# Kernel optimization log

Hardware: AMD Instinct MI355X
Metric: run time of the kernel (lower is better)

The kernel has to match this reference:

```python
import jax, jax.numpy as jnp
import numpy as np

N_NODES = 10000
N_EDGES = 640000
D = 128
N_LAYERS = 4


def setup_inputs() -> dict:
    key = jax.random.key(0)
    k1, k2, k3, k4, k5 = jax.random.split(key, 5)
    node_feats = jax.random.normal(k1, (N_NODES, D), dtype=jnp.float32)
    src = jax.random.randint(k2, (N_EDGES,), 0, N_NODES, dtype=jnp.int32)
    dst = jax.random.randint(k3, (N_EDGES,), 0, N_NODES, dtype=jnp.int32)
    # stacked per-layer Linear params (all layers are 128 -> 128)
    Ws = jax.random.normal(k4, (N_LAYERS, D, D), dtype=jnp.float32) / np.sqrt(D).astype(np.float32)
    bs = jax.random.normal(k5, (N_LAYERS, D), dtype=jnp.float32) * 0.01
    return {"node_feats": node_feats, "src": src, "dst": dst, "Ws": Ws, "bs": bs}


def reference(node_feats, src, dst, Ws, bs):
    # Each GCN_layer: h = Linear(x); h = sum_{u in N(v)} h_u  (copy_u/sum)
    # dgl.add_self_loop => aggregate includes the node's own h, i.e. + h.
    # activation = relu; dropout is identity in eval; no batchnorm / residual.
    def step(h, params):
        W, b = params
        hl = h @ W + b                                   # [N, D] dense GEMM
        msgs = hl[src]                                   # [E, D] gather
        agg = jax.ops.segment_sum(msgs, dst, num_segments=N_NODES) + hl  # scatter-sum + self-loop
        return jax.nn.relu(agg), None

    h, _ = jax.lax.scan(step, node_feats, (Ws, bs))
    return h
```

## Files before the change

### kernel.cpp

```cpp
#include <hip/hip_runtime.h>
#include <hip/hip_bf16.h>

#define N_NODES 10000
#define N_EDGES 640000
#define D 128
#define N_LAYERS 4

#define NBINS 79
#define BIN_CAP 10240
#define POISON 0xAAAAAAAAu
#define A_LD 136

typedef unsigned uv4 __attribute__((ext_vector_type(4)));
typedef short bf16x8 __attribute__((ext_vector_type(8)));
typedef float f32x4 __attribute__((ext_vector_type(4)));
typedef float f32x2 __attribute__((ext_vector_type(2)));


__global__ __launch_bounds__(256) void binA_wt_kernel(const int* __restrict__ src,
                                                      const int* __restrict__ dst,
                                                      unsigned* __restrict__ binCursor,
                                                      unsigned* __restrict__ binbuf,
                                                      const float* __restrict__ W,
                                                      unsigned short* __restrict__ Wt) {
    __shared__ int cnt[NBINS];
    __shared__ int gbase[NBINS];
    const int t = threadIdx.x;
    const int b = blockIdx.x;

    if (b >= 250) {
        const int g = (b - 250) * 256 + t;
        const int e0 = g * 8;
        const int l = e0 >> 14;
        const int r = e0 & 16383;
        const int n = r >> 7;
        const int k0 = r & 127;
        union { bf16x8 v; __hip_bfloat16 h[8]; } pk;
#pragma unroll
        for (int j = 0; j < 8; ++j)
            pk.h[j] = __float2bfloat16(W[l * 16384 + (k0 + j) * 128 + n]);
        *(bf16x8*)(Wt + e0) = pk.v;
        return;
    }

    if (t < NBINS) cnt[t] = 0;
    __syncthreads();

    const int e0 = b * 2560;
    unsigned key[10];
    int bin[10], pos[10];
#pragma unroll
    for (int j = 0; j < 10; ++j) {
        int e = e0 + j * 256 + t;
        int d = dst[e];
        int s = src[e];
        key[j] = ((unsigned)d << 14) | (unsigned)s;
        bin[j] = d >> 7;
        pos[j] = atomicAdd(&cnt[bin[j]], 1);
    }
    __syncthreads();
    if (t < NBINS) {
        unsigned old = atomicAdd(&binCursor[t], (unsigned)cnt[t]);
        gbase[t] = (int)(old - POISON);
    }
    __syncthreads();
#pragma unroll
    for (int j = 0; j < 10; ++j) {
        int p = gbase[bin[j]] + pos[j];
        if (p >= 0 && p < BIN_CAP) binbuf[bin[j] * BIN_CAP + p] = key[j];
    }
}

__global__ __launch_bounds__(256) void binB_kernel(unsigned* __restrict__ binbuf,
                                                   const unsigned* __restrict__ binCursor,
                                                   int* __restrict__ begs,
                                                   int* __restrict__ degs) {
    __shared__ unsigned buf[BIN_CAP];
    __shared__ int deg[128], base[128], cur[128];
    const int b = blockIdx.x;
    const int t = threadIdx.x;
    int m = (int)(binCursor[b] - POISON);
    if (m > BIN_CAP) m = BIN_CAP;
    if (m < 0) m = 0;

    if (t < 128) deg[t] = 0;
    __syncthreads();

    for (int i = t; i < m; i += 256) {
        unsigned k = binbuf[(size_t)b * BIN_CAP + i];
        buf[i] = k;
        atomicAdd(&deg[(k >> 14) & 127], 1);
    }
    __syncthreads();

    if (t < 64) {
        int a0 = deg[2 * t], a1 = deg[2 * t + 1];
        int s = a0 + a1;
        int x = s;
#pragma unroll
        for (int off = 1; off < 64; off <<= 1) {
            int tt = __shfl_up(x, off);
            if (t >= off) x += tt;
        }
        base[2 * t]     = x - s;
        base[2 * t + 1] = x - a1;
        cur[2 * t]      = x - s;
        cur[2 * t + 1]  = x - a1;
    }
    __syncthreads();

    if (t < 128) {
        int v = b * 128 + t;
        if (v < N_NODES) {
            degs[v] = deg[t];
            begs[v] = b * BIN_CAP + base[t];
        }
    }

    for (int i = t; i < m; i += 256) {
        unsigned k = buf[i];
        int p = atomicAdd(&cur[(k >> 14) & 127], 1);
        binbuf[(size_t)b * BIN_CAP + p] = k & 0x3FFFu;
    }
}


__global__ __launch_bounds__(256) void gemm0_kernel(const float* __restrict__ hf,
                                                    const unsigned short* __restrict__ WtL,
                                                    const float* __restrict__ bias,
                                                    unsigned short* __restrict__ hl) {
    const int t = threadIdx.x;
    const int wave = t >> 6;
    const int lane = t & 63;
    const int ln = lane & 15;
    const int q = lane >> 4;
    const int row0 = blockIdx.x * 64 + wave * 16;

    int m = row0 + ln;
    if (m > N_NODES - 1) m = N_NODES - 1;

    f32x4 acc[8];
#pragma unroll
    for (int n0 = 0; n0 < 8; ++n0) acc[n0] = (f32x4){0.f, 0.f, 0.f, 0.f};

#pragma unroll
    for (int k0 = 0; k0 < 128; k0 += 32) {
        float4 f0 = *(const float4*)(hf + (size_t)m * D + k0 + q * 8);
        float4 f1 = *(const float4*)(hf + (size_t)m * D + k0 + q * 8 + 4);
        union { bf16x8 v; __hip_bfloat16 b[8]; } pk;
        pk.b[0] = __float2bfloat16(f0.x); pk.b[1] = __float2bfloat16(f0.y);
        pk.b[2] = __float2bfloat16(f0.z); pk.b[3] = __float2bfloat16(f0.w);
        pk.b[4] = __float2bfloat16(f1.x); pk.b[5] = __float2bfloat16(f1.y);
        pk.b[6] = __float2bfloat16(f1.z); pk.b[7] = __float2bfloat16(f1.w);
        bf16x8 a = pk.v;
#pragma unroll
        for (int n0 = 0; n0 < 8; ++n0) {
            bf16x8 bb = *(const bf16x8*)(WtL + (size_t)(n0 * 16 + ln) * D + k0 + q * 8);
            acc[n0] = __builtin_amdgcn_mfma_f32_16x16x32_bf16(a, bb, acc[n0], 0, 0, 0);
        }
    }

#pragma unroll
    for (int n0 = 0; n0 < 8; ++n0) {
        float bv = bias[n0 * 16 + ln];
#pragma unroll
        for (int r = 0; r < 4; ++r) {
            int row = row0 + q * 4 + r;
            if (row < N_NODES) {
                __hip_bfloat16 o = __float2bfloat16(acc[n0][r] + bv);
                hl[(size_t)row * D + n0 * 16 + ln] = *(unsigned short*)&o;
            }
        }
    }
}

__device__ __forceinline__ float bf_lo(unsigned u) {
    u <<= 16; return __builtin_bit_cast(float, u);
}
__device__ __forceinline__ float bf_hi(unsigned u) {
    u &= 0xffff0000u; return __builtin_bit_cast(float, u);
}
__device__ __forceinline__ f32x2 bf_pair(unsigned u) {
    return (f32x2){bf_lo(u), bf_hi(u)};
}

__device__ __forceinline__ void agg_rows(int node, const uv4* __restrict__ hlq,
                                         const int* __restrict__ begs,
                                         const int* __restrict__ degs,
                                         const int* __restrict__ csr,
                                         f32x2& a0, f32x2& a1, f32x2& a2, f32x2& a3) {
    const int lane = threadIdx.x & 63;
    const int g = lane >> 4;
    const int c = lane & 15;

    const int beg = begs[node];
    const int end = beg + degs[node];

    a0 = (f32x2){0.f, 0.f}; a1 = a0; a2 = a0; a3 = a0;
    if (g == 0) {
        uv4 sv = hlq[node * 16 + c];
        a0 = bf_pair(sv.x); a1 = bf_pair(sv.y);
        a2 = bf_pair(sv.z); a3 = bf_pair(sv.w);
    }

    for (int eb = beg; eb < end; eb += 64) {
        int ce = eb + lane;
        int cv = csr[ce < end ? ce : (end - 1)];
#pragma unroll
        for (int half = 0; half < 2; ++half) {
            int b0 = eb + 32 * half;
            if (b0 < end) {
#pragma unroll
                for (int j = 0; j < 8; ++j) {
                    int e0 = b0 + 4 * j;
                    if (e0 < end) {
                        int e = e0 + g;
                        int u = __shfl(cv, 32 * half + 4 * j + g);
                        uv4 v = hlq[u * 16 + c];
                        if (e >= end) { v.x = 0u; v.y = 0u; v.z = 0u; v.w = 0u; }
                        a0 += bf_pair(v.x);
                        a1 += bf_pair(v.y);
                        a2 += bf_pair(v.z);
                        a3 += bf_pair(v.w);
                    }
                }
            }
        }
    }

#pragma unroll
    for (int off = 16; off <= 32; off <<= 1) {
        a0.x += __shfl_xor(a0.x, off); a0.y += __shfl_xor(a0.y, off);
        a1.x += __shfl_xor(a1.x, off); a1.y += __shfl_xor(a1.y, off);
        a2.x += __shfl_xor(a2.x, off); a2.y += __shfl_xor(a2.y, off);
        a3.x += __shfl_xor(a3.x, off); a3.y += __shfl_xor(a3.y, off);
    }
}

__global__ __launch_bounds__(1024, 8) void agg_gemm_kernel(
        const uv4* __restrict__ hlq, const int* __restrict__ begs,
        const int* __restrict__ degs, const int* __restrict__ csr,
        const unsigned short* __restrict__ WtL, const float* __restrict__ bias,
        unsigned short* __restrict__ hlo) {
    __shared__ __hip_bfloat16 Arow[16 * A_LD];
    const int t = threadIdx.x;
    const int wave = t >> 6;
    const int lane = t & 63;
    const int g = lane >> 4;
    const int c = lane & 15;
    const int node = blockIdx.x * 16 + wave;

    f32x2 a0, a1, a2, a3;
    agg_rows(node, hlq, begs, degs, csr, a0, a1, a2, a3);

    if (g == 0) {
        union { bf16x8 v; __hip_bfloat16 h[8]; } pk;
        pk.h[0] = __float2bfloat16(fmaxf(a0.x, 0.f));
        pk.h[1] = __float2bfloat16(fmaxf(a0.y, 0.f));
        pk.h[2] = __float2bfloat16(fmaxf(a1.x, 0.f));
        pk.h[3] = __float2bfloat16(fmaxf(a1.y, 0.f));
        pk.h[4] = __float2bfloat16(fmaxf(a2.x, 0.f));
        pk.h[5] = __float2bfloat16(fmaxf(a2.y, 0.f));
        pk.h[6] = __float2bfloat16(fmaxf(a3.x, 0.f));
        pk.h[7] = __float2bfloat16(fmaxf(a3.y, 0.f));
        *(bf16x8*)&Arow[wave * A_LD + c * 8] = pk.v;
    }
    __syncthreads();

    if (wave < 8) {
        const int ln = lane & 15;
        const int q = lane >> 4;
        f32x4 acc = (f32x4){0.f, 0.f, 0.f, 0.f};
#pragma unroll
        for (int k0 = 0; k0 < 128; k0 += 32) {
            bf16x8 a = *(const bf16x8*)&Arow[ln * A_LD + k0 + q * 8];
            bf16x8 bb = *(const bf16x8*)(WtL + (size_t)(wave * 16 + ln) * D + k0 + q * 8);
            acc = __builtin_amdgcn_mfma_f32_16x16x32_bf16(a, bb, acc, 0, 0, 0);
        }
        float bv = bias[wave * 16 + ln];
#pragma unroll
        for (int r = 0; r < 4; ++r) {
            int row = blockIdx.x * 16 + q * 4 + r;
            __hip_bfloat16 o = __float2bfloat16(acc[r] + bv);
            hlo[(size_t)row * D + wave * 16 + ln] = *(unsigned short*)&o;
        }
    }
}

__global__ __launch_bounds__(256) void agg_final_kernel(const uv4* __restrict__ hlq,
                                                        const int* __restrict__ begs,
                                                        const int* __restrict__ degs,
                                                        const int* __restrict__ csr,
                                                        float* __restrict__ outf) {
    int node = blockIdx.x * 4 + (threadIdx.x >> 6);
    if (node >= N_NODES) return;
    const int lane = threadIdx.x & 63;
    const int g = lane >> 4;
    const int c = lane & 15;

    f32x2 a0, a1, a2, a3;
    agg_rows(node, hlq, begs, degs, csr, a0, a1, a2, a3);

    if (g == 0) {
        float4 o0, o1;
        o0.x = fmaxf(a0.x, 0.f); o0.y = fmaxf(a0.y, 0.f);
        o0.z = fmaxf(a1.x, 0.f); o0.w = fmaxf(a1.y, 0.f);
        o1.x = fmaxf(a2.x, 0.f); o1.y = fmaxf(a2.y, 0.f);
        o1.z = fmaxf(a3.x, 0.f); o1.w = fmaxf(a3.y, 0.f);
        float4* orow = (float4*)(outf + (size_t)node * D);
        orow[c * 2]     = o0;
        orow[c * 2 + 1] = o1;
    }
}


extern "C" void kernel_launch(void* const* d_in, const int* in_sizes, int n_in,
                              void* d_out, int out_size, void* d_ws, size_t ws_size,
                              hipStream_t stream) {
    const float* node_feats = (const float*)d_in[0];
    const int*   src        = (const int*)d_in[1];
    const int*   dst        = (const int*)d_in[2];
    const float* Ws         = (const float*)d_in[3];
    const float* bs         = (const float*)d_in[4];
    float* out = (float*)d_out;

    char* ws = (char*)d_ws;
    unsigned* binCursor     = (unsigned*)(ws + 0);
    int*      begs          = (int*)(ws + 1024);
    int*      degs          = (int*)(ws + 41984);
    unsigned* binbuf        = (unsigned*)(ws + 82944);
    unsigned short* hlA     = (unsigned short*)(ws + 3318784);
    unsigned short* hlB     = (unsigned short*)(ws + 5878784);
    unsigned short* Wt      = (unsigned short*)(ws + 8438784);
    const int* csr = (const int*)binbuf;

    binA_wt_kernel<<<282, 256, 0, stream>>>(src, dst, binCursor, binbuf, Ws, Wt);
    binB_kernel<<<NBINS, 256, 0, stream>>>(binbuf, binCursor, begs, degs);

    gemm0_kernel<<<157, 256, 0, stream>>>(node_feats, Wt, bs, hlA);
    agg_gemm_kernel<<<625, 1024, 0, stream>>>((const uv4*)hlA, begs, degs, csr,
                                              Wt + 1 * 16384, bs + 1 * D, hlB);
    agg_gemm_kernel<<<625, 1024, 0, stream>>>((const uv4*)hlB, begs, degs, csr,
                                              Wt + 2 * 16384, bs + 2 * D, hlA);
    agg_gemm_kernel<<<625, 1024, 0, stream>>>((const uv4*)hlA, begs, degs, csr,
                                              Wt + 3 * 16384, bs + 3 * D, hlB);
    agg_final_kernel<<<2500, 256, 0, stream>>>((const uv4*)hlB, begs, degs, csr, out);
}
```

Baseline: 173.6 us.

## Merge bin sort and first GEMM into one launch; prefetch next CSR chunk

Merges the binB CSR-building kernel and the layer-0 GEMM into one grid: the extra blocks beyond NBINS run the GEMM, which does not depend on the binning. This removes one kernel launch and lets the two independent stages run concurrently. Separately, the aggregation loop software-prefetches the next 64-entry chunk of neighbor indices before processing the current one. The GEMM blocks now reserve the 40KB shared buffer they do not use, which may reduce occupancy.

```diff
diff --git a/kernel.cpp b/kernel.cpp
--- a/kernel.cpp
+++ b/kernel.cpp
@@ -71,14 +71,63 @@
     }
 }
 
-__global__ __launch_bounds__(256) void binB_kernel(unsigned* __restrict__ binbuf,
-                                                   const unsigned* __restrict__ binCursor,
-                                                   int* __restrict__ begs,
-                                                   int* __restrict__ degs) {
+
+__global__ __launch_bounds__(256) void binB_gemm0_kernel(
+        unsigned* __restrict__ binbuf, const unsigned* __restrict__ binCursor,
+        int* __restrict__ begs, int* __restrict__ degs,
+        const float* __restrict__ hf, const unsigned short* __restrict__ WtL,
+        const float* __restrict__ bias, unsigned short* __restrict__ hl) {
     __shared__ unsigned buf[BIN_CAP];
     __shared__ int deg[128], base[128], cur[128];
     const int b = blockIdx.x;
     const int t = threadIdx.x;
+
+    if (b >= NBINS) {
+        const int wave = t >> 6;
+        const int lane = t & 63;
+        const int ln = lane & 15;
+        const int q = lane >> 4;
+        const int row0 = (b - NBINS) * 64 + wave * 16;
+
+        int m = row0 + ln;
+        if (m > N_NODES - 1) m = N_NODES - 1;
+
+        f32x4 acc[8];
+#pragma unroll
+        for (int n0 = 0; n0 < 8; ++n0) acc[n0] = (f32x4){0.f, 0.f, 0.f, 0.f};
+
+#pragma unroll
+        for (int k0 = 0; k0 < 128; k0 += 32) {
+            float4 f0 = *(const float4*)(hf + (size_t)m * D + k0 + q * 8);
+            float4 f1 = *(const float4*)(hf + (size_t)m * D + k0 + q * 8 + 4);
+            union { bf16x8 v; __hip_bfloat16 b8[8]; } pk;
+            pk.b8[0] = __float2bfloat16(f0.x); pk.b8[1] = __float2bfloat16(f0.y);
+            pk.b8[2] = __float2bfloat16(f0.z); pk.b8[3] = __float2bfloat16(f0.w);
+            pk.b8[4] = __float2bfloat16(f1.x); pk.b8[5] = __float2bfloat16(f1.y);
+            pk.b8[6] = __float2bfloat16(f1.z); pk.b8[7] = __float2bfloat16(f1.w);
+            bf16x8 a = pk.v;
+#pragma unroll
+            for (int n0 = 0; n0 < 8; ++n0) {
+                bf16x8 bb = *(const bf16x8*)(WtL + (size_t)(n0 * 16 + ln) * D + k0 + q * 8);
+                acc[n0] = __builtin_amdgcn_mfma_f32_16x16x32_bf16(a, bb, acc[n0], 0, 0, 0);
+            }
+        }
+
+#pragma unroll
+        for (int n0 = 0; n0 < 8; ++n0) {
+            float bv = bias[n0 * 16 + ln];
+#pragma unroll
+            for (int r = 0; r < 4; ++r) {
+                int row = row0 + q * 4 + r;
+                if (row < N_NODES) {
+                    __hip_bfloat16 o = __float2bfloat16(acc[n0][r] + bv);
+                    hl[(size_t)row * D + n0 * 16 + ln] = *(unsigned short*)&o;
+                }
+            }
+        }
+        return;
+    }
+
     int m = (int)(binCursor[b] - POISON);
     if (m > BIN_CAP) m = BIN_CAP;
     if (m < 0) m = 0;
@@ -121,56 +170,6 @@
         unsigned k = buf[i];
         int p = atomicAdd(&cur[(k >> 14) & 127], 1);
         binbuf[(size_t)b * BIN_CAP + p] = k & 0x3FFFu;
-    }
-}
-
-
-__global__ __launch_bounds__(256) void gemm0_kernel(const float* __restrict__ hf,
-                                                    const unsigned short* __restrict__ WtL,
-                                                    const float* __restrict__ bias,
-                                                    unsigned short* __restrict__ hl) {
-    const int t = threadIdx.x;
-    const int wave = t >> 6;
-    const int lane = t & 63;
-    const int ln = lane & 15;
-    const int q = lane >> 4;
-    const int row0 = blockIdx.x * 64 + wave * 16;
-
-    int m = row0 + ln;
-    if (m > N_NODES - 1) m = N_NODES - 1;
-
-    f32x4 acc[8];
-#pragma unroll
-    for (int n0 = 0; n0 < 8; ++n0) acc[n0] = (f32x4){0.f, 0.f, 0.f, 0.f};
-
-#pragma unroll
-    for (int k0 = 0; k0 < 128; k0 += 32) {
-        float4 f0 = *(const float4*)(hf + (size_t)m * D + k0 + q * 8);
-        float4 f1 = *(const float4*)(hf + (size_t)m * D + k0 + q * 8 + 4);
-        union { bf16x8 v; __hip_bfloat16 b[8]; } pk;
-        pk.b[0] = __float2bfloat16(f0.x); pk.b[1] = __float2bfloat16(f0.y);
-        pk.b[2] = __float2bfloat16(f0.z); pk.b[3] = __float2bfloat16(f0.w);
-        pk.b[4] = __float2bfloat16(f1.x); pk.b[5] = __float2bfloat16(f1.y);
-        pk.b[6] = __float2bfloat16(f1.z); pk.b[7] = __float2bfloat16(f1.w);
-        bf16x8 a = pk.v;
-#pragma unroll
-        for (int n0 = 0; n0 < 8; ++n0) {
-            bf16x8 bb = *(const bf16x8*)(WtL + (size_t)(n0 * 16 + ln) * D + k0 + q * 8);
-            acc[n0] = __builtin_amdgcn_mfma_f32_16x16x32_bf16(a, bb, acc[n0], 0, 0, 0);
-        }
-    }
-
-#pragma unroll
-    for (int n0 = 0; n0 < 8; ++n0) {
-        float bv = bias[n0 * 16 + ln];
-#pragma unroll
-        for (int r = 0; r < 4; ++r) {
-            int row = row0 + q * 4 + r;
-            if (row < N_NODES) {
-                __hip_bfloat16 o = __float2bfloat16(acc[n0][r] + bv);
-                hl[(size_t)row * D + n0 * 16 + ln] = *(unsigned short*)&o;
-            }
-        }
     }
 }
 
@@ -203,9 +202,14 @@
         a2 = bf_pair(sv.z); a3 = bf_pair(sv.w);
     }
 
+    int ce0 = beg + lane;
+    int cvn = csr[ce0 < end ? ce0 : (end - 1)];
     for (int eb = beg; eb < end; eb += 64) {
-        int ce = eb + lane;
-        int cv = csr[ce < end ? ce : (end - 1)];
+        int cv = cvn;
+        if (eb + 64 < end) {
+            int cen = eb + 64 + lane;
+            cvn = csr[cen < end ? cen : (end - 1)];
+        }
 #pragma unroll
         for (int half = 0; half < 2; ++half) {
             int b0 = eb + 32 * half;
@@ -335,9 +339,8 @@
     const int* csr = (const int*)binbuf;
 
     binA_wt_kernel<<<282, 256, 0, stream>>>(src, dst, binCursor, binbuf, Ws, Wt);
-    binB_kernel<<<NBINS, 256, 0, stream>>>(binbuf, binCursor, begs, degs);
-
-    gemm0_kernel<<<157, 256, 0, stream>>>(node_feats, Wt, bs, hlA);
+    binB_gemm0_kernel<<<NBINS + 157, 256, 0, stream>>>(binbuf, binCursor, begs, degs,
+                                                       node_feats, Wt, bs, hlA);
     agg_gemm_kernel<<<625, 1024, 0, stream>>>((const uv4*)hlA, begs, degs, csr,
                                               Wt + 1 * 16384, bs + 1 * D, hlB);
     agg_gemm_kernel<<<625, 1024, 0, stream>>>((const uv4*)hlB, begs, degs, csr,
```

After: 162.9 us. 1.07x faster.
